# Kernel tuning notes

Measured on AMD Instinct MI355X. Metric: run time of the kernel, lower is better.

Reference implementation:

```python
import jax, jax.numpy as jnp
import numpy as np

EPS = 1e-4
B, C_IN, H, W = 64, 512, 14, 14
P, NCLS = 2000, 200


def setup_inputs() -> dict:
    key = jax.random.key(0)
    k1, k2 = jax.random.split(key)
    x = jax.random.normal(k1, (B, C_IN, H, W), dtype=jnp.float32)
    prototype_vectors = jax.random.uniform(k2, (P, C_IN, 1, 1), dtype=jnp.float32)
    # fc weight init: +1 for the prototype's own class, -0.5 otherwise
    per_class = P // NCLS
    assoc = (np.arange(P) // per_class)[:, None] == np.arange(NCLS)[None, :]  # [P, NCLS]
    assoc = assoc.astype(np.float32)
    fc_weight = jnp.asarray(1.0 * assoc.T - 0.5 * (1.0 - assoc.T))  # [NCLS, P]
    return {"x": x, "prototype_vectors": prototype_vectors, "fc_weight": fc_weight}


def reference(x, prototype_vectors, fc_weight):
    # prototypes are 1x1, so the conv is a channel contraction
    p = prototype_vectors[:, :, 0, 0]  # [P, C]
    xp = jnp.einsum('bchw,pc->bphw', x, p)                 # cross term
    x2_patch_sum = jnp.sum(x * x, axis=1, keepdims=True)   # [B,1,H,W] (ones-kernel conv, identical across P)
    p2 = jnp.sum(p * p, axis=1)[None, :, None, None]       # [1,P,1,1]
    dists = jax.nn.relu(x2_patch_sum - 2.0 * xp + p2)      # [B,P,H,W]
    min_dists = jnp.min(dists, axis=(2, 3))                # global min-pool -> [B,P]
    activations = jnp.log((min_dists + 1.0) / (min_dists + EPS))
    logits = activations @ fc_weight.T                     # [B,NCLS]
    return (x, min_dists, dists, activations, logits)
```

## Files before the change

kernel.cpp:

```cpp
#include <hip/hip_runtime.h>
#include <math.h>


#define EPSV 1e-4f
typedef unsigned short ushort_t;

constexpr int NB  = 64;
constexpr int NC  = 512;
constexpr int NHW = 196;
constexpr int NP  = 2000;
constexpr int NPAD = 2048;
constexpr int NCL = 200;
constexpr int MM   = NB * NHW;
constexpr int XTOT = NB * NC * NHW;

constexpr long long OFF_MIN = XTOT;
constexpr long long OFF_D   = OFF_MIN + (long long)NB * NP;
constexpr long long OFF_ACT = OFF_D + (long long)NB * NP * NHW;
constexpr long long OFF_LOG = OFF_ACT + (long long)NB * NP;

typedef __attribute__((ext_vector_type(8))) short short8;
typedef __attribute__((ext_vector_type(4))) float f32x4;

__device__ __forceinline__ unsigned bf16rne(float f) {
    unsigned u = __float_as_uint(f);
    return (u + 0x7FFFu + ((u >> 16) & 1u)) >> 16;
}

__device__ __forceinline__ void gl_lds16(const void* g, void* l) {
    __builtin_amdgcn_global_load_lds(
        (const __attribute__((address_space(1))) unsigned int*)g,
        (__attribute__((address_space(3))) unsigned int*)l, 16, 0, 0);
}

__global__ __launch_bounds__(256) void splitp_kernel(const float* __restrict__ proto,
                              ushort_t* __restrict__ ph, float* __restrict__ p2,
                              float* __restrict__ mind, float* __restrict__ x2) {
    int gi = blockIdx.x * 256 + threadIdx.x;
    if (gi < NB * NP) mind[gi] = 3.402823466e38f;
    if (gi < MM)      x2[gi]  = 0.f;

    int p = blockIdx.x * 4 + (threadIdx.x >> 6);
    int l = threadIdx.x & 63;
    unsigned hs[8];
    float s = 0.f;
    if (p < NP) {
        const float4* pr = (const float4*)(proto + (size_t)p * NC + l * 8);
        float4 a = pr[0], bb = pr[1];
        float vv[8] = {a.x, a.y, a.z, a.w, bb.x, bb.y, bb.z, bb.w};
        #pragma unroll
        for (int k = 0; k < 8; ++k) { hs[k] = bf16rne(vv[k]); s += vv[k] * vv[k]; }
    } else {
        #pragma unroll
        for (int k = 0; k < 8; ++k) hs[k] = 0;
    }
    uint4 H = make_uint4(hs[0] | (hs[1] << 16), hs[2] | (hs[3] << 16),
                         hs[4] | (hs[5] << 16), hs[6] | (hs[7] << 16));
    int col = (l >> 3) * 64 + (((l & 7) ^ (p & 7)) << 3);
    *(uint4*)&ph[(size_t)p * NC + col] = H;
    for (int off = 32; off; off >>= 1) s += __shfl_down(s, off, 64);
    if (l == 0) p2[p] = s;
}

__global__ __launch_bounds__(256) void splitx_kernel(const float* __restrict__ x,
                                                     ushort_t* __restrict__ xh,
                                                     float* __restrict__ x2) {
    __shared__ float tl[64 * 197];
    const int b = blockIdx.x >> 3, cc = blockIdx.x & 7;
    const int c0 = cc * 64;
    const float* src = x + ((size_t)b * NC + c0) * NHW;
    for (int idx = threadIdx.x; idx < 64 * 196; idx += 256)
        tl[(idx / 196) * 197 + (idx % 196)] = src[idx];
    __syncthreads();
    for (int idx = threadIdx.x; idx < 1568; idx += 256) {
        int hw = idx >> 3, slot = idx & 7;
        int m = b * 196 + hw;
        unsigned hs[8];
        #pragma unroll
        for (int e = 0; e < 8; ++e)
            hs[e] = bf16rne(tl[(slot * 8 + e) * 197 + hw]);
        uint4 H = make_uint4(hs[0] | (hs[1] << 16), hs[2] | (hs[3] << 16),
                             hs[4] | (hs[5] << 16), hs[6] | (hs[7] << 16));
        *(uint4*)&xh[(size_t)m * NC + c0 + ((slot ^ (m & 7)) << 3)] = H;
    }
    if (threadIdx.x < 196) {
        float s = 0.f;
        #pragma unroll 8
        for (int cl = 0; cl < 64; ++cl) { float v = tl[cl * 197 + threadIdx.x]; s += v * v; }
        atomicAdd(&x2[b * 196 + threadIdx.x], s);
    }
}

__global__ __launch_bounds__(256) void gemm_kernel(
    const ushort_t* __restrict__ xh, const ushort_t* __restrict__ ph,
    const float* __restrict__ p2, const float* __restrict__ x2,
    float* __restrict__ dists, unsigned* __restrict__ mind)
{
    __shared__ ushort_t Ah[128 * 64];
    __shared__ ushort_t Bh[128 * 64];

    const int wg  = blockIdx.x;
    const int swz = (wg & 7) * 196 + (wg >> 3);
    const int nt  = swz / 98, mt = swz - nt * 98;

    const int t = threadIdx.x;
    const int lane = t & 63, lm = lane & 15, kg = lane >> 4;
    const int w = t >> 6, wp = w >> 1, wx = w & 1;

    const size_t ga = (size_t)(mt * 128 + (t >> 3)) * NC + (t & 7) * 8;
    const size_t gb = (size_t)(nt * 128 + (t >> 3)) * NC + (t & 7) * 8;
    const size_t gs = (size_t)32 * NC;

    f32x4 acc[4][4];
    #pragma unroll
    for (int i = 0; i < 4; ++i)
        #pragma unroll
        for (int j = 0; j < 4; ++j) acc[i][j] = 0.f;

    for (int c0 = 0; c0 < NC; c0 += 64) {
        #pragma unroll
        for (int q = 0; q < 4; ++q) {
            gl_lds16(xh + ga + q * gs + c0, &Ah[q * 2048 + t * 8]);
            gl_lds16(ph + gb + q * gs + c0, &Bh[q * 2048 + t * 8]);
        }
        __syncthreads();

        short8 PF[2][4], XF[2][4];
        #pragma unroll
        for (int s = 0; s < 2; ++s)
            #pragma unroll
            for (int i = 0; i < 4; ++i) {
                int prow = wp * 64 + i * 16 + lm;
                int xrow = wx * 64 + i * 16 + lm;
                int lsp = (s * 4 + kg) ^ (prow & 7);
                int lsx = (s * 4 + kg) ^ (xrow & 7);
                PF[s][i] = *(const short8*)&Bh[prow * 64 + lsp * 8];
                XF[s][i] = *(const short8*)&Ah[xrow * 64 + lsx * 8];
            }
        #pragma unroll
        for (int s = 0; s < 2; ++s)
            #pragma unroll
            for (int i = 0; i < 4; ++i)
                #pragma unroll
                for (int j = 0; j < 4; ++j)
                    acc[i][j] = __builtin_amdgcn_mfma_f32_16x16x32_bf16(PF[s][i], XF[s][j], acc[i][j], 0, 0, 0);
        __syncthreads();
    }

    const int mhalf = mt * 128 + wx * 64;
    const int b0h = mhalf / 196;
    const int b1h = (mhalf + 63) / 196;
    float x2v[4]; int bj[4]; size_t dbase[4];
    #pragma unroll
    for (int j = 0; j < 4; ++j) {
        int m = mhalf + j * 16 + lm;
        x2v[j] = x2[m];
        int b = m / 196, hw = m - b * 196;
        bj[j] = b;
        dbase[j] = (size_t)b * ((size_t)NP * NHW) + hw;
    }
    #pragma unroll
    for (int i = 0; i < 4; ++i) {
        #pragma unroll
        for (int r = 0; r < 4; ++r) {
            int p = nt * 128 + wp * 64 + i * 16 + kg * 4 + r;
            if (p < NP) {
                float p2v = p2[p];
                float mn0 = 3.402823466e38f, mn1 = 3.402823466e38f;
                #pragma unroll
                for (int j = 0; j < 4; ++j) {
                    float v = fmaxf(x2v[j] - 2.f * acc[i][j][r] + p2v, 0.f);
                    __builtin_nontemporal_store(v, &dists[dbase[j] + (size_t)p * NHW]);
                    if (bj[j] == b0h) mn0 = fminf(mn0, v); else mn1 = fminf(mn1, v);
                }
                #pragma unroll
                for (int off = 1; off < 16; off <<= 1) {
                    mn0 = fminf(mn0, __shfl_xor(mn0, off, 64));
                    mn1 = fminf(mn1, __shfl_xor(mn1, off, 64));
                }
                if (lm == 0) {
                    atomicMin(&mind[b0h * NP + p], __float_as_uint(mn0));
                    if (b1h != b0h) atomicMin(&mind[b1h * NP + p], __float_as_uint(mn1));
                }
            }
        }
    }
}

__global__ void act_kernel(const float* __restrict__ mind, float* __restrict__ act) {
    int i = blockIdx.x * 256 + threadIdx.x;
    if (i < NB * NP) { float md = mind[i]; act[i] = logf((md + 1.f) / (md + EPSV)); }
}

__global__ void logits_kernel(const float* __restrict__ act,
                              const float* __restrict__ fc, float* __restrict__ out) {
    int r = blockIdx.x * 4 + (threadIdx.x >> 6);
    int l = threadIdx.x & 63;
    int b = r / NCL, n = r - b * NCL;
    const float* arow = act + b * NP;
    const float* frow = fc + n * NP;
    float s = 0.f;
    for (int k = l; k < NP; k += 64) s += arow[k] * frow[k];
    for (int off = 32; off; off >>= 1) s += __shfl_down(s, off, 64);
    if (l == 0) out[r] = s;
}

__global__ void copy_kernel(const f32x4* __restrict__ in, f32x4* __restrict__ out, int n4) {
    for (int i = blockIdx.x * blockDim.x + threadIdx.x; i < n4; i += gridDim.x * blockDim.x) {
        f32x4 v = __builtin_nontemporal_load(&in[i]);
        __builtin_nontemporal_store(v, &out[i]);
    }
}

extern "C" void kernel_launch(void* const* d_in, const int* in_sizes, int n_in,
                              void* d_out, int out_size, void* d_ws, size_t ws_size,
                              hipStream_t stream) {
    const float* x     = (const float*)d_in[0];
    const float* proto = (const float*)d_in[1];
    const float* fc    = (const float*)d_in[2];
    float* out = (float*)d_out;

    ushort_t* xh = (ushort_t*)out;
    ushort_t* ph = (ushort_t*)d_ws;
    float*    p2 = (float*)(ph + (size_t)NPAD * NC);
    float*    x2 = p2 + NPAD;

    float* mind  = out + OFF_MIN;
    float* dists = out + OFF_D;
    float* act   = out + OFF_ACT;
    float* logit = out + OFF_LOG;

    splitp_kernel<<<512, 256, 0, stream>>>(proto, ph, p2, mind, x2);
    splitx_kernel<<<512, 256, 0, stream>>>(x, xh, x2);

    gemm_kernel<<<1568, 256, 0, stream>>>(xh, ph, p2, x2, dists, (unsigned*)mind);

    act_kernel<<<500, 256, 0, stream>>>(mind, act);
    logits_kernel<<<3200, 256, 0, stream>>>(act, fc, logit);

    copy_kernel<<<2048, 256, 0, stream>>>((const f32x4*)x, (f32x4*)out, XTOT / 4);
}
```

Baseline: 262.6 us.

## Double-buffer GEMM LDS tiles and fuse x passthrough copy into split kernel

Double-buffers the LDS tiles in the GEMM so the next K-slice loads overlap MFMA work on the current slice, leaving one barrier per step. When the workspace is large enough, the bf16 copy of x goes into the workspace instead of the output buffer, so the split kernel can write the fp32 passthrough of x directly and the separate copy kernel is skipped. This saves a full reread of x but doubles LDS use per block, which may lower occupancy, and the copy path now depends on workspace size.

```diff
diff --git a/kernel.cpp b/kernel.cpp
--- a/kernel.cpp
+++ b/kernel.cpp
@@ -64,13 +64,19 @@
 
 __global__ __launch_bounds__(256) void splitx_kernel(const float* __restrict__ x,
                                                      ushort_t* __restrict__ xh,
-                                                     float* __restrict__ x2) {
+                                                     float* __restrict__ x2,
+                                                     float* __restrict__ xcopy,
+                                                     int do_copy) {
     __shared__ float tl[64 * 197];
     const int b = blockIdx.x >> 3, cc = blockIdx.x & 7;
     const int c0 = cc * 64;
-    const float* src = x + ((size_t)b * NC + c0) * NHW;
-    for (int idx = threadIdx.x; idx < 64 * 196; idx += 256)
-        tl[(idx / 196) * 197 + (idx % 196)] = src[idx];
+    const size_t gbase = ((size_t)b * NC + c0) * NHW;
+    const float* src = x + gbase;
+    for (int idx = threadIdx.x; idx < 64 * 196; idx += 256) {
+        float v = src[idx];
+        tl[(idx / 196) * 197 + (idx % 196)] = v;
+        if (do_copy) __builtin_nontemporal_store(v, &xcopy[gbase + idx]);
+    }
     __syncthreads();
     for (int idx = threadIdx.x; idx < 1568; idx += 256) {
         int hw = idx >> 3, slot = idx & 7;
@@ -96,8 +102,8 @@
     const float* __restrict__ p2, const float* __restrict__ x2,
     float* __restrict__ dists, unsigned* __restrict__ mind)
 {
-    __shared__ ushort_t Ah[128 * 64];
-    __shared__ ushort_t Bh[128 * 64];
+    __shared__ ushort_t Ah[2][128 * 64];
+    __shared__ ushort_t Bh[2][128 * 64];
 
     const int wg  = blockIdx.x;
     const int swz = (wg & 7) * 196 + (wg >> 3);
@@ -111,19 +117,25 @@
     const size_t gb = (size_t)(nt * 128 + (t >> 3)) * NC + (t & 7) * 8;
     const size_t gs = (size_t)32 * NC;
 
+#define STAGE(bufi, c0) do {                                            \
+        _Pragma("unroll")                                               \
+        for (int q = 0; q < 4; ++q) {                                   \
+            gl_lds16(xh + ga + q * gs + (c0), &Ah[bufi][q * 2048 + t * 8]); \
+            gl_lds16(ph + gb + q * gs + (c0), &Bh[bufi][q * 2048 + t * 8]); \
+        } } while (0)
+
     f32x4 acc[4][4];
     #pragma unroll
     for (int i = 0; i < 4; ++i)
         #pragma unroll
         for (int j = 0; j < 4; ++j) acc[i][j] = 0.f;
 
-    for (int c0 = 0; c0 < NC; c0 += 64) {
-        #pragma unroll
-        for (int q = 0; q < 4; ++q) {
-            gl_lds16(xh + ga + q * gs + c0, &Ah[q * 2048 + t * 8]);
-            gl_lds16(ph + gb + q * gs + c0, &Bh[q * 2048 + t * 8]);
-        }
-        __syncthreads();
+    STAGE(0, 0);
+    __syncthreads();
+
+    for (int step = 0; step < 8; ++step) {
+        const int cur = step & 1;
+        if (step < 7) STAGE(cur ^ 1, (step + 1) * 64);
 
         short8 PF[2][4], XF[2][4];
         #pragma unroll
@@ -134,8 +146,8 @@
                 int xrow = wx * 64 + i * 16 + lm;
                 int lsp = (s * 4 + kg) ^ (prow & 7);
                 int lsx = (s * 4 + kg) ^ (xrow & 7);
-                PF[s][i] = *(const short8*)&Bh[prow * 64 + lsp * 8];
-                XF[s][i] = *(const short8*)&Ah[xrow * 64 + lsx * 8];
+                PF[s][i] = *(const short8*)&Bh[cur][prow * 64 + lsp * 8];
+                XF[s][i] = *(const short8*)&Ah[cur][xrow * 64 + lsx * 8];
             }
         #pragma unroll
         for (int s = 0; s < 2; ++s)
@@ -146,6 +158,7 @@
                     acc[i][j] = __builtin_amdgcn_mfma_f32_16x16x32_bf16(PF[s][i], XF[s][j], acc[i][j], 0, 0, 0);
         __syncthreads();
     }
+#undef STAGE
 
     const int mhalf = mt * 128 + wx * 64;
     const int b0h = mhalf / 196;
@@ -220,10 +233,14 @@
     const float* fc    = (const float*)d_in[2];
     float* out = (float*)d_out;
 
-    ushort_t* xh = (ushort_t*)out;
     ushort_t* ph = (ushort_t*)d_ws;
     float*    p2 = (float*)(ph + (size_t)NPAD * NC);
     float*    x2 = p2 + NPAD;
+    ushort_t* xh_ws = (ushort_t*)(x2 + MM);
+    const size_t ws_need = (size_t)NPAD * NC * 2 + NPAD * 4 + MM * 4 + (size_t)XTOT * 2;
+    const bool xh_in_ws = ws_size >= ws_need;
+
+    ushort_t* xh = xh_in_ws ? xh_ws : (ushort_t*)out;
 
     float* mind  = out + OFF_MIN;
     float* dists = out + OFF_D;
@@ -231,12 +248,13 @@
     float* logit = out + OFF_LOG;
 
     splitp_kernel<<<512, 256, 0, stream>>>(proto, ph, p2, mind, x2);
-    splitx_kernel<<<512, 256, 0, stream>>>(x, xh, x2);
+    splitx_kernel<<<512, 256, 0, stream>>>(x, xh, x2, out, xh_in_ws ? 1 : 0);
 
     gemm_kernel<<<1568, 256, 0, stream>>>(xh, ph, p2, x2, dists, (unsigned*)mind);
 
     act_kernel<<<500, 256, 0, stream>>>(mind, act);
     logits_kernel<<<3200, 256, 0, stream>>>(act, fc, logit);
 
-    copy_kernel<<<2048, 256, 0, stream>>>((const f32x4*)x, (f32x4*)out, XTOT / 4);
-}
+    if (!xh_in_ws)
+        copy_kernel<<<2048, 256, 0, stream>>>((const f32x4*)x, (f32x4*)out, XTOT / 4);
+}
```

After: 277.7 us. +5.8%, slower.
